# Kernel tuning notes

Measured on AMD Instinct MI355X. Metric: run time of the kernel, lower is better.

## Reference

```python
import jax, jax.numpy as jnp
import numpy as np

BIG, SMALL = 13, 3
NK = 5                       # ceil(BIG / SMALL)
PADDING = SMALL - 1          # 2
EXTRA_PAD = PADDING - SMALL // 2   # 1
G = 2                        # group_in
C_OUT = 96
C_IN = G * C_OUT * NK        # 960
B, H, W = 16, 56, 56


def setup_inputs() -> dict:
    key = jax.random.key(0)
    k1, k2 = jax.random.split(key, 2)
    rng = np.random.default_rng(0)
    mid = BIG // 2
    real_pad = np.array([mid - i * SMALL - PADDING for i in range(NK)], dtype=np.int32)  # [4,1,-2,-5,-8]

    def perm_pads():
        # per output channel, a random permutation of the nk shift offsets
        return np.concatenate([rng.permutation(real_pad) for _ in range(C_OUT)])

    ph = np.stack([perm_pads() for _ in range(G)])  # (G, C_OUT*NK) horizontal shifts
    pv = np.stack([perm_pads() for _ in range(G)])  # (G, C_OUT*NK) vertical shifts
    pad_hv = np.concatenate([ph, pv], axis=0).T.astype(np.int32)  # (C_OUT*NK, 2*G)

    ids = []
    for _ in range(G):
        col = []
        for _ in range(C_OUT):
            arr = -np.ones(NK, dtype=np.int32)
            pos = rng.choice(NK, min(4, NK), replace=False)
            arr[pos] = np.arange(min(4, NK))
            col.append(arr)
        ids.append(np.concatenate(col))
    idx_identit = np.stack(ids).T.astype(np.int32)  # (C_OUT*NK, G)

    x = jax.random.normal(k1, (B, C_IN, H, W), jnp.float32)
    proj_w = jax.random.normal(k2, (C_OUT, C_IN), jnp.float32) * np.float32(1.0 / np.sqrt(C_IN))
    return {
        'x': x,
        'pad_hv': jnp.asarray(pad_hv),
        'idx_identit': jnp.asarray(idx_identit),
        'local_scale': jnp.ones((1, C_IN, 1, 1), jnp.float32),
        'local_bias': jnp.zeros((1, C_IN, 1, 1), jnp.float32),
        'proj_w': proj_w,
        'fuse_alpha': jnp.float32(0.7),
        'b': B, 'hout': H, 'wout': W,
    }


def reference(x, pad_hv, idx_identit, local_scale, local_bias, proj_w, fuse_alpha, b, hout, wout):
    p = EXTRA_PAD
    xp = jnp.pad(x, ((0, 0), (0, 0), (p, p), (p, p)), mode='edge')  # replicate pad
    Bx, Cin, Hp, Wp = xp.shape

    # per-channel shift offsets: channel ic = g*C_OUT*NK + slot, slot = co*NK + k
    ph = pad_hv[:, :G].T.reshape(-1)  # (C_IN,) horizontal (w-axis) shifts
    pv = pad_hv[:, G:].T.reshape(-1)  # (C_IN,) vertical (h-axis) shifts

    def gather_w(xc, s):  # xc: (B, Hp, Wp), s: scalar int shift
        idx = jnp.arange(wout) + p + s
        valid = ((idx >= 0) & (idx < Wp)).astype(xc.dtype)
        return xc[:, p:p + hout, jnp.clip(idx, 0, Wp - 1)] * valid[None, None, :]

    def gather_h(xc, s):
        idx = jnp.arange(hout) + p + s
        valid = ((idx >= 0) & (idx < Hp)).astype(xc.dtype)
        return xc[:, jnp.clip(idx, 0, Hp - 1), p:p + wout] * valid[None, :, None]

    xh = jax.vmap(gather_w, in_axes=(1, 0), out_axes=1)(xp, ph)  # (B, C_IN, hout, wout)
    xv = jax.vmap(gather_h, in_axes=(1, 0), out_axes=1)(xp, pv)
    x1 = xh.reshape(Bx, G, C_OUT, NK, hout, wout).sum((1, 3))    # horizontal-shift group
    x2 = xv.reshape(Bx, G, C_OUT, NK, hout, wout).sum((1, 3))    # vertical-shift group

    id_mask = (idx_identit.T.reshape(-1) >= 0).astype(xp.dtype)  # (C_IN,) identity slots
    x3 = (xp[:, :, p:p + hout, p:p + wout] * id_mask[None, :, None, None])
    x3 = x3.reshape(Bx, G, C_OUT, NK, hout, wout).sum((1, 3))    # identity group

    global_feat = (x1 + x2 + x3) / 3.0

    local = xp * (local_scale + 1e-5) + local_bias
    local = jax.image.resize(local, (Bx, Cin, hout, wout), method='bilinear')  # align_corners=False
    local = jnp.einsum('bchw,oc->bohw', local, proj_w)  # 1x1 conv, no bias

    return fuse_alpha * global_feat + (1.0 - fuse_alpha) * local
```

## Files before the change

kernel.cpp:

```cpp
#include <hip/hip_runtime.h>
#include <hip/hip_bf16.h>
#include <cstdint>
#include <cstddef>

#define B_    16
#define CIN   960
#define HH    56
#define WW_   56
#define GG    2
#define COUT  96
#define NK_   5
#define PIX   3136
#define NCH   30

#define WF_OFF   0
#define BIAS_OFF 61440
#define Y_OFF    61568

typedef __attribute__((ext_vector_type(8))) short bf16x8;
typedef __attribute__((ext_vector_type(4))) float f32x4;

__device__ __forceinline__ short f2b(float f) {
    union { float f; unsigned u; } c; c.f = f;
    unsigned r = (c.u + 0x7FFFu + ((c.u >> 16) & 1u)) >> 16;
    return (short)r;
}
__device__ __forceinline__ float b2f(short s) {
    union { unsigned u; float f; } c;
    c.u = ((unsigned)(unsigned short)s) << 16;
    return c.f;
}

#define GLOAD_LDS16(gp, lp)                                                        \
    __builtin_amdgcn_global_load_lds(                                              \
        (const __attribute__((address_space(1))) unsigned*)(gp),                   \
        (__attribute__((address_space(3))) unsigned*)(lp), 16, 0, 0)

__global__ void prep_wb(const float* __restrict__ pw, const float* __restrict__ sc,
                        short* __restrict__ wf) {
    int idx = blockIdx.x * 256 + threadIdx.x;
    if (idx >= NCH * 6 * 64) return;
    const int lane = idx & 63;
    const int nf   = idx >> 6;
    const int f    = nf % 6;
    const int n    = nf / 6;
    const int o    = f * 16 + (lane & 15);
    const int c0   = n * 32 + (lane >> 4) * 8;
    bf16x8 v;
#pragma unroll
    for (int k = 0; k < 8; ++k)
        v[k] = f2b(pw[o * CIN + c0 + k] * (sc[c0 + k] + 1e-5f));
    *(bf16x8*)((char*)wf + (size_t)n * 8192 + (f * 64 + lane) * 16) = v;
}

__global__ void prep_bias(const float* __restrict__ pw, const float* __restrict__ bi,
                          float* __restrict__ bias) {
    const int o = blockIdx.x;
    const int l = threadIdx.x;
    float s = 0.f;
    for (int c = l; c < CIN; c += 64) s += pw[o * CIN + c] * bi[c];
#pragma unroll
    for (int off = 32; off; off >>= 1) s += __shfl_down(s, off);
    if (l == 0) bias[o] = s;
}

__global__ __launch_bounds__(512)
void conv_mfma(const float* __restrict__ x, const short* __restrict__ wf,
               short* __restrict__ yb) {
    const int tid  = threadIdx.x;
    const int lane = tid & 63;
    const int wv   = tid >> 6;
    const int m    = wv >> 2;
    const int n    = wv & 3;
    const int b    = blockIdx.y;
    const int px0  = blockIdx.x * 64;

    __shared__ __align__(16) char xsb[3 * 8192];
    __shared__ __align__(16) char wlb[3 * 8192];

    const float* xbase = x + (size_t)b * CIN * PIX + px0;
    const char*  wfB   = (const char*)wf;

    const int sch  = wv * 4 + (lane >> 4);
    const int sS   = (wv >> 1) & 3;
    const int soff = (((lane >> 2) & 3) ^ sS) * 16 + (lane & 3) * 4;
    const int wsub = wv * 1024 + lane * 16;

    const int kb    = lane >> 4;
    const int bcol  = (lane & 15) * 4;
    const int bslot = ((n ^ kb) & 3) * 64;
    const int babs  = kb * 2048 + bslot + bcol;
    const int abase = m * 3072 + lane * 16;

    f32x4 acc0 = {0.f, 0.f, 0.f, 0.f};
    f32x4 acc1 = {0.f, 0.f, 0.f, 0.f};
    f32x4 acc2 = {0.f, 0.f, 0.f, 0.f};

#define STAGE(BS, c0)                                                            \
    {                                                                            \
        GLOAD_LDS16(xbase + (size_t)((c0) + sch) * PIX + soff,                   \
                    xsb + (BS) * 8192 + wv * 1024);                              \
        GLOAD_LDS16(wfB + (size_t)((c0) >> 5) * 8192 + wsub,                     \
                    wlb + (BS) * 8192 + wv * 1024);                              \
    }

    STAGE(0, 0);
    STAGE(1, 32);

#define STEP(n_, BI, BS, VM)                                                     \
    {                                                                            \
        asm volatile("s_waitcnt vmcnt(" #VM ")" ::: "memory");                   \
        asm volatile("s_barrier" ::: "memory");                                  \
        bf16x8 bfrag;                                                            \
        _Pragma("unroll")                                                        \
        for (int k = 0; k < 8; ++k)                                              \
            bfrag[k] = f2b(*(const float*)(xsb + (BI) * 8192 + babs + k * 256)); \
        const bf16x8 af0 = *(const bf16x8*)(wlb + (BI) * 8192 + abase);          \
        const bf16x8 af1 = *(const bf16x8*)(wlb + (BI) * 8192 + abase + 1024);   \
        const bf16x8 af2 = *(const bf16x8*)(wlb + (BI) * 8192 + abase + 2048);   \
        if ((n_) + 2 < NCH) STAGE(BS, ((n_) + 2) * 32);                          \
        acc0 = __builtin_amdgcn_mfma_f32_16x16x32_bf16(af0, bfrag, acc0, 0,0,0); \
        acc1 = __builtin_amdgcn_mfma_f32_16x16x32_bf16(af1, bfrag, acc1, 0,0,0); \
        acc2 = __builtin_amdgcn_mfma_f32_16x16x32_bf16(af2, bfrag, acc2, 0,0,0); \
    }

#pragma unroll 1
    for (int mm = 0; mm < 9; ++mm) {
        const int n0 = mm * 3;
        STEP(n0 + 0, 0, 2, 2);
        STEP(n0 + 1, 1, 0, 2);
        STEP(n0 + 2, 2, 1, 2);
    }
    STEP(27, 0, 2, 2);
    STEP(28, 1, 0, 2);
    STEP(29, 2, 1, 0);
#undef STEP
#undef STAGE

    short* yp = yb + (size_t)b * COUT * PIX + px0 + n * 16 + (lane & 15);
    const int o0 = m * 48 + (lane >> 4) * 4;
#pragma unroll
    for (int r = 0; r < 4; ++r) yp[(size_t)(o0 +      r) * PIX] = f2b(acc0[r]);
#pragma unroll
    for (int r = 0; r < 4; ++r) yp[(size_t)(o0 + 16 + r) * PIX] = f2b(acc1[r]);
#pragma unroll
    for (int r = 0; r < 4; ++r) yp[(size_t)(o0 + 32 + r) * PIX] = f2b(acc2[r]);
}

__device__ __forceinline__ void rweights56(int o, short* idx, float* wt) {
    const float ratio = 58.0f / 56.0f;
    const float kinv  = 56.0f / 58.0f;
    const float sf = ((float)o + 0.5f) * ratio - 0.5f;
    const int f0 = (int)floorf(sf);
    float sum = 0.f;
#pragma unroll
    for (int t = 0; t < 4; ++t) {
        int i = f0 - 1 + t;
        float w = fmaxf(1.0f - fabsf(sf - (float)i) * kinv, 0.0f);
        if (i < 0 || i > 57) w = 0.0f;
        idx[t] = (short)min(HH - 1, max(0, i - 1));
        wt[t] = w;
        sum += w;
    }
    const float inv = 1.0f / sum;
#pragma unroll
    for (int t = 0; t < 4; ++t) wt[t] *= inv;
}

__global__ __launch_bounds__(256)
void finalize(const float* __restrict__ x, const int* __restrict__ pad_hv,
              const int* __restrict__ idt, const short* __restrict__ yb,
              const float* __restrict__ bias, const float* __restrict__ alpha_p,
              float* __restrict__ out) {
    const int bc = blockIdx.x;
    const int co = bc % COUT;
    const int b  = bc / COUT;
    const int t  = threadIdx.x;

    __shared__ float  ylds[PIX];
    __shared__ float4 wt4[56];
    __shared__ short4 id4[56];
    __shared__ int   ish[10], isv[10], ipl[10];
    __shared__ float fid[10];

    if (t < 10) {
        const int g = t / 5;
        const int k = t - g * 5;
        const int slot = co * NK_ + k;
        ish[t] = pad_hv[slot * 4 + g];
        isv[t] = pad_hv[slot * 4 + 2 + g];
        fid[t] = (idt[slot * 2 + g] >= 0) ? 1.f : 0.f;
        ipl[t] = (g * (COUT * NK_) + slot) * PIX;
    }
    if (t < 56) {
        short ii[4]; float ww[4];
        rweights56(t, ii, ww);
        wt4[t] = make_float4(ww[0], ww[1], ww[2], ww[3]);
        id4[t] = make_short4(ii[0], ii[1], ii[2], ii[3]);
    }
    {
        const short* yp = yb + (size_t)bc * PIX;
#pragma unroll 1
        for (int i = t; i < PIX / 4; i += 256) {
            const short4 s4 = *(const short4*)(yp + i * 4);
            *(float4*)(ylds + i * 4) =
                make_float4(b2f(s4.x), b2f(s4.y), b2f(s4.z), b2f(s4.w));
        }
    }
    __syncthreads();

    int   ish_r[10], isv_r[10], ipl_r[10];
    float fid_r[10];
#pragma unroll
    for (int p = 0; p < 10; ++p) {
        ish_r[p] = ish[p]; isv_r[p] = isv[p];
        ipl_r[p] = ipl[p]; fid_r[p] = fid[p];
    }

    const float alpha = alpha_p[0];
    const float ia    = 1.0f - alpha;
    const float bco   = bias[co];
    const float* xb = x + (size_t)b * CIN * PIX;
    float* op = out + (size_t)bc * PIX;

#pragma unroll 1
    for (int px = t; px < PIX; px += 256) {
        const int h = (px * 18725) >> 20;
        const int w = px - h * WW_;
        const int hrow = px - w;

        float accg = 0.f;
#pragma unroll
        for (int p = 0; p < 10; ++p) {
            const float* xc = xb + ipl_r[p];
            const int jw = w + ish_r[p];
            const float mh = (jw >= -1 && jw <= WW_) ? 1.f : 0.f;
            accg += mh * xc[hrow + min(WW_ - 1, max(0, jw))];

            const int iv = h + isv_r[p];
            const float mv = (iv >= -1 && iv <= HH) ? 1.f : 0.f;
            accg += mv * xc[min(HH - 1, max(0, iv)) * WW_ + w];

            accg += fid_r[p] * xc[px];
        }

        const float4 ww4 = wt4[w];
        const short4 iw4 = id4[w];
        const float4 wh4 = wt4[h];
        const short4 ih4 = id4[h];
        float accl = 0.f;
#pragma unroll
        for (int a = 0; a < 4; ++a) {
            const int row = ((const short*)&ih4)[a] * WW_;
            const float* yr = ylds + row;
            float rs;
            rs = ww4.x * yr[iw4.x];
            rs = fmaf(ww4.y, yr[iw4.y], rs);
            rs = fmaf(ww4.z, yr[iw4.z], rs);
            rs = fmaf(ww4.w, yr[iw4.w], rs);
            accl = fmaf(((const float*)&wh4)[a], rs, accl);
        }
        accl += bco;

        op[px] = alpha * accg * (1.0f / 3.0f) + ia * accl;
    }
}

extern "C" void kernel_launch(void* const* d_in, const int* in_sizes, int n_in,
                              void* d_out, int out_size, void* d_ws, size_t ws_size,
                              hipStream_t stream) {
    const float* x      = (const float*)d_in[0];
    const int*   pad_hv = (const int*)d_in[1];
    const int*   idt    = (const int*)d_in[2];
    const float* lsc    = (const float*)d_in[3];
    const float* lbi    = (const float*)d_in[4];
    const float* pw     = (const float*)d_in[5];
    const float* alpha  = (const float*)d_in[6];
    float* out = (float*)d_out;

    float* ws   = (float*)d_ws;
    short* wf   = (short*)(ws + WF_OFF);
    float* bias = ws + BIAS_OFF;
    short* yb   = (short*)(ws + Y_OFF);

    prep_wb<<<(NCH * 6 * 64 + 255) / 256, 256, 0, stream>>>(pw, lsc, wf);
    prep_bias<<<COUT, 64, 0, stream>>>(pw, lbi, bias);
    conv_mfma<<<dim3(PIX / 64, B_), 512, 0, stream>>>(x, wf, yb);
    finalize<<<B_ * COUT, 256, 0, stream>>>(x, pad_hv, idt, yb, bias, alpha, out);
}
```

Before: 93.50 us.

## Register-prefetch x, convert once to bf16 in LDS, double-buffer 64-channel phases

```diff
diff --git a/kernel.cpp b/kernel.cpp
--- a/kernel.cpp
+++ b/kernel.cpp
@@ -12,6 +12,7 @@
 #define NK_   5
 #define PIX   3136
 #define NCH   30
+#define NPH   15
 
 #define WF_OFF   0
 #define BIAS_OFF 61440
@@ -75,67 +76,83 @@
     const int b    = blockIdx.y;
     const int px0  = blockIdx.x * 64;
 
-    __shared__ __align__(16) char xsb[3 * 8192];
-    __shared__ __align__(16) char wlb[3 * 8192];
-
-    const float* xbase = x + (size_t)b * CIN * PIX + px0;
+    __shared__ __align__(16) char xls[2 * 8192];
+    __shared__ __align__(16) char wls[2 * 16384];
+
+    const float* xbase = x + (size_t)b * CIN * PIX + px0 + lane;
     const char*  wfB   = (const char*)wf;
 
-    const int sch  = wv * 4 + (lane >> 4);
-    const int sS   = (wv >> 1) & 3;
-    const int soff = (((lane >> 2) & 3) ^ sS) * 16 + (lane & 3) * 4;
-    const int wsub = wv * 1024 + lane * 16;
-
-    const int kb    = lane >> 4;
-    const int bcol  = (lane & 15) * 4;
-    const int bslot = ((n ^ kb) & 3) * 64;
-    const int babs  = kb * 2048 + bslot + bcol;
+    const int ssub = (wv >> 2) * 4096 + (wv & 3) * 1024 + lane * 16;
+    const int sc0  = (wv >> 2) * 32 + (wv & 3) * 8;
+    const int bbase = (lane >> 4) * 1024 + (n * 16 + (lane & 15)) * 16;
     const int abase = m * 3072 + lane * 16;
 
     f32x4 acc0 = {0.f, 0.f, 0.f, 0.f};
     f32x4 acc1 = {0.f, 0.f, 0.f, 0.f};
     f32x4 acc2 = {0.f, 0.f, 0.f, 0.f};
 
-#define STAGE(BS, c0)                                                            \
-    {                                                                            \
-        GLOAD_LDS16(xbase + (size_t)((c0) + sch) * PIX + soff,                   \
-                    xsb + (BS) * 8192 + wv * 1024);                              \
-        GLOAD_LDS16(wfB + (size_t)((c0) >> 5) * 8192 + wsub,                     \
-                    wlb + (BS) * 8192 + wv * 1024);                              \
-    }
-
-    STAGE(0, 0);
-    STAGE(1, 32);
-
-#define STEP(n_, BI, BS, VM)                                                     \
-    {                                                                            \
-        asm volatile("s_waitcnt vmcnt(" #VM ")" ::: "memory");                   \
-        asm volatile("s_barrier" ::: "memory");                                  \
-        bf16x8 bfrag;                                                            \
+    float vA[8], vB[8];
+
+#define XLOAD(DST, P)                                                            \
+    {                                                                            \
         _Pragma("unroll")                                                        \
         for (int k = 0; k < 8; ++k)                                              \
-            bfrag[k] = f2b(*(const float*)(xsb + (BI) * 8192 + babs + k * 256)); \
-        const bf16x8 af0 = *(const bf16x8*)(wlb + (BI) * 8192 + abase);          \
-        const bf16x8 af1 = *(const bf16x8*)(wlb + (BI) * 8192 + abase + 1024);   \
-        const bf16x8 af2 = *(const bf16x8*)(wlb + (BI) * 8192 + abase + 2048);   \
-        if ((n_) + 2 < NCH) STAGE(BS, ((n_) + 2) * 32);                          \
-        acc0 = __builtin_amdgcn_mfma_f32_16x16x32_bf16(af0, bfrag, acc0, 0,0,0); \
-        acc1 = __builtin_amdgcn_mfma_f32_16x16x32_bf16(af1, bfrag, acc1, 0,0,0); \
-        acc2 = __builtin_amdgcn_mfma_f32_16x16x32_bf16(af2, bfrag, acc2, 0,0,0); \
-    }
+            DST[k] = xbase[(size_t)((P) * 64 + sc0 + k) * PIX];                  \
+    }
+#define WLOAD(P)                                                                 \
+    {                                                                            \
+        _Pragma("unroll")                                                        \
+        for (int s = 0; s < 2; ++s)                                              \
+            GLOAD_LDS16(wfB + (size_t)(2 * (P) + s) * 8192 + wv * 1024 + lane * 16, \
+                        wls + ((P) & 1) * 16384 + s * 8192 + wv * 1024);         \
+    }
+#define PACKWRITE(CUR, P)                                                        \
+    {                                                                            \
+        bf16x8 pk;                                                               \
+        _Pragma("unroll")                                                        \
+        for (int k = 0; k < 8; ++k) pk[k] = f2b(CUR[k]);                         \
+        *(bf16x8*)(xls + ((P) & 1) * 8192 + ssub) = pk;                          \
+    }
+#define COMPUTE(P)                                                               \
+    {                                                                            \
+        _Pragma("unroll")                                                        \
+        for (int s = 0; s < 2; ++s) {                                            \
+            const bf16x8 bf = *(const bf16x8*)(xls + ((P) & 1) * 8192 + s * 4096 + bbase); \
+            const char* wb_ = wls + ((P) & 1) * 16384 + s * 8192 + abase;        \
+            const bf16x8 a0 = *(const bf16x8*)(wb_);                             \
+            const bf16x8 a1 = *(const bf16x8*)(wb_ + 1024);                      \
+            const bf16x8 a2 = *(const bf16x8*)(wb_ + 2048);                      \
+            acc0 = __builtin_amdgcn_mfma_f32_16x16x32_bf16(a0, bf, acc0, 0,0,0); \
+            acc1 = __builtin_amdgcn_mfma_f32_16x16x32_bf16(a1, bf, acc1, 0,0,0); \
+            acc2 = __builtin_amdgcn_mfma_f32_16x16x32_bf16(a2, bf, acc2, 0,0,0); \
+        }                                                                        \
+    }
+#define PHASE(P, CUR, NXT, VM, ISSUE)                                            \
+    {                                                                            \
+        if (ISSUE) XLOAD(NXT, (P) + 1);                                          \
+        asm volatile("s_waitcnt vmcnt(" #VM ")" ::: "memory");                   \
+        PACKWRITE(CUR, P);                                                       \
+        asm volatile("s_waitcnt lgkmcnt(0)" ::: "memory");                       \
+        asm volatile("s_barrier" ::: "memory");                                  \
+        if (ISSUE) WLOAD((P) + 1);                                               \
+        COMPUTE(P);                                                              \
+    }
+
+    XLOAD(vA, 0);
+    WLOAD(0);
 
 #pragma unroll 1
-    for (int mm = 0; mm < 9; ++mm) {
-        const int n0 = mm * 3;
-        STEP(n0 + 0, 0, 2, 2);
-        STEP(n0 + 1, 1, 0, 2);
-        STEP(n0 + 2, 2, 1, 2);
-    }
-    STEP(27, 0, 2, 2);
-    STEP(28, 1, 0, 2);
-    STEP(29, 2, 1, 0);
-#undef STEP
-#undef STAGE
+    for (int pp = 0; pp < 7; ++pp) {
+        const int p0 = pp * 2;
+        PHASE(p0 + 0, vA, vB, 8, 1);
+        PHASE(p0 + 1, vB, vA, 8, 1);
+    }
+    PHASE(14, vA, vB, 0, 0);
+#undef PHASE
+#undef COMPUTE
+#undef PACKWRITE
+#undef WLOAD
+#undef XLOAD
 
     short* yp = yb + (size_t)b * COUT * PIX + px0 + n * 16 + (lane & 15);
     const int o0 = m * 48 + (lane >> 4) * 4;
```

Result: slower. 102.1 us (+9.2%).

## Replace LDS-staged triple buffering with direct register double-buffered global loads

Applied to the files above, without the earlier changes.

```diff
diff --git a/kernel.cpp b/kernel.cpp
--- a/kernel.cpp
+++ b/kernel.cpp
@@ -30,11 +30,6 @@
     c.u = ((unsigned)(unsigned short)s) << 16;
     return c.f;
 }
-
-#define GLOAD_LDS16(gp, lp)                                                        \
-    __builtin_amdgcn_global_load_lds(                                              \
-        (const __attribute__((address_space(1))) unsigned*)(gp),                   \
-        (__attribute__((address_space(3))) unsigned*)(lp), 16, 0, 0)
 
 __global__ void prep_wb(const float* __restrict__ pw, const float* __restrict__ sc,
                         short* __restrict__ wf) {
@@ -75,67 +70,59 @@
     const int b    = blockIdx.y;
     const int px0  = blockIdx.x * 64;
 
-    __shared__ __align__(16) char xsb[3 * 8192];
-    __shared__ __align__(16) char wlb[3 * 8192];
-
-    const float* xbase = x + (size_t)b * CIN * PIX + px0;
-    const char*  wfB   = (const char*)wf;
-
-    const int sch  = wv * 4 + (lane >> 4);
-    const int sS   = (wv >> 1) & 3;
-    const int soff = (((lane >> 2) & 3) ^ sS) * 16 + (lane & 3) * 4;
-    const int wsub = wv * 1024 + lane * 16;
-
-    const int kb    = lane >> 4;
-    const int bcol  = (lane & 15) * 4;
-    const int bslot = ((n ^ kb) & 3) * 64;
-    const int babs  = kb * 2048 + bslot + bcol;
-    const int abase = m * 3072 + lane * 16;
+    const float* xpx = x + (size_t)b * CIN * PIX + px0 + n * 16 + (lane & 15);
+    const int kb8 = (lane >> 4) * 8;
+    const char* wfl = (const char*)wf + m * 3072 + lane * 16;
 
     f32x4 acc0 = {0.f, 0.f, 0.f, 0.f};
     f32x4 acc1 = {0.f, 0.f, 0.f, 0.f};
     f32x4 acc2 = {0.f, 0.f, 0.f, 0.f};
 
-#define STAGE(BS, c0)                                                            \
+    float  xA[8], xB[8];
+    bf16x8 wA0, wA1, wA2, wB0, wB1, wB2;
+
+#define LOADX(DST, N)                                                            \
     {                                                                            \
-        GLOAD_LDS16(xbase + (size_t)((c0) + sch) * PIX + soff,                   \
-                    xsb + (BS) * 8192 + wv * 1024);                              \
-        GLOAD_LDS16(wfB + (size_t)((c0) >> 5) * 8192 + wsub,                     \
-                    wlb + (BS) * 8192 + wv * 1024);                              \
-    }
-
-    STAGE(0, 0);
-    STAGE(1, 32);
-
-#define STEP(n_, BI, BS, VM)                                                     \
-    {                                                                            \
-        asm volatile("s_waitcnt vmcnt(" #VM ")" ::: "memory");                   \
-        asm volatile("s_barrier" ::: "memory");                                  \
-        bf16x8 bfrag;                                                            \
         _Pragma("unroll")                                                        \
         for (int k = 0; k < 8; ++k)                                              \
-            bfrag[k] = f2b(*(const float*)(xsb + (BI) * 8192 + babs + k * 256)); \
-        const bf16x8 af0 = *(const bf16x8*)(wlb + (BI) * 8192 + abase);          \
-        const bf16x8 af1 = *(const bf16x8*)(wlb + (BI) * 8192 + abase + 1024);   \
-        const bf16x8 af2 = *(const bf16x8*)(wlb + (BI) * 8192 + abase + 2048);   \
-        if ((n_) + 2 < NCH) STAGE(BS, ((n_) + 2) * 32);                          \
-        acc0 = __builtin_amdgcn_mfma_f32_16x16x32_bf16(af0, bfrag, acc0, 0,0,0); \
-        acc1 = __builtin_amdgcn_mfma_f32_16x16x32_bf16(af1, bfrag, acc1, 0,0,0); \
-        acc2 = __builtin_amdgcn_mfma_f32_16x16x32_bf16(af2, bfrag, acc2, 0,0,0); \
-    }
+            DST[k] = xpx[(size_t)((N) * 32 + kb8 + k) * PIX];                    \
+    }
+#define LOADW(D0, D1, D2, N)                                                     \
+    {                                                                            \
+        const char* wp_ = wfl + (size_t)(N) * 8192;                              \
+        D0 = *(const bf16x8*)(wp_);                                              \
+        D1 = *(const bf16x8*)(wp_ + 1024);                                       \
+        D2 = *(const bf16x8*)(wp_ + 2048);                                       \
+    }
+#define COMP(XV, W0, W1, W2)                                                     \
+    {                                                                            \
+        bf16x8 bf;                                                               \
+        _Pragma("unroll")                                                        \
+        for (int k = 0; k < 8; ++k) bf[k] = f2b(XV[k]);                          \
+        acc0 = __builtin_amdgcn_mfma_f32_16x16x32_bf16(W0, bf, acc0, 0, 0, 0);   \
+        acc1 = __builtin_amdgcn_mfma_f32_16x16x32_bf16(W1, bf, acc1, 0, 0, 0);   \
+        acc2 = __builtin_amdgcn_mfma_f32_16x16x32_bf16(W2, bf, acc2, 0, 0, 0);   \
+    }
+
+    LOADX(xA, 0);
+    LOADW(wA0, wA1, wA2, 0);
 
 #pragma unroll 1
-    for (int mm = 0; mm < 9; ++mm) {
-        const int n0 = mm * 3;
-        STEP(n0 + 0, 0, 2, 2);
-        STEP(n0 + 1, 1, 0, 2);
-        STEP(n0 + 2, 2, 1, 2);
-    }
-    STEP(27, 0, 2, 2);
-    STEP(28, 1, 0, 2);
-    STEP(29, 2, 1, 0);
-#undef STEP
-#undef STAGE
+    for (int p = 0; p < 14; ++p) {
+        LOADX(xB, 2 * p + 1);
+        LOADW(wB0, wB1, wB2, 2 * p + 1);
+        COMP(xA, wA0, wA1, wA2);
+        LOADX(xA, 2 * p + 2);
+        LOADW(wA0, wA1, wA2, 2 * p + 2);
+        COMP(xB, wB0, wB1, wB2);
+    }
+    LOADX(xB, 29);
+    LOADW(wB0, wB1, wB2, 29);
+    COMP(xA, wA0, wA1, wA2);
+    COMP(xB, wB0, wB1, wB2);
+#undef COMP
+#undef LOADW
+#undef LOADX
 
     short* yp = yb + (size_t)b * COUT * PIX + px0 + n * 16 + (lane & 15);
     const int o0 = m * 48 + (lane >> 4) * 4;
```

Result: slower. 121.0 us (+29.4%).

## Load activations to registers, convert once to bf16 in LDS, DMA weights separately

Applied to the files above, without the earlier changes.

```diff
diff --git a/kernel.cpp b/kernel.cpp
--- a/kernel.cpp
+++ b/kernel.cpp
@@ -75,67 +75,84 @@
     const int b    = blockIdx.y;
     const int px0  = blockIdx.x * 64;
 
-    __shared__ __align__(16) char xsb[3 * 8192];
-    __shared__ __align__(16) char wlb[3 * 8192];
-
-    const float* xbase = x + (size_t)b * CIN * PIX + px0;
-    const char*  wfB   = (const char*)wf;
-
-    const int sch  = wv * 4 + (lane >> 4);
-    const int sS   = (wv >> 1) & 3;
-    const int soff = (((lane >> 2) & 3) ^ sS) * 16 + (lane & 3) * 4;
+    __shared__ __align__(16) char xls[2 * 4096];
+    __shared__ __align__(16) char wls[3 * 8192];
+
+    const int skb = wv >> 1;
+    const int sh8 = (wv & 1) * 8;
+    const float* xsrc = x + (size_t)b * CIN * PIX + px0 + lane
+                        + (size_t)(skb * 8 + (wv & 1) * 4) * PIX;
+    const int wxb = skb * 1024 + lane * 16 + sh8;
+    const char* wfB = (const char*)wf;
     const int wsub = wv * 1024 + lane * 16;
 
-    const int kb    = lane >> 4;
-    const int bcol  = (lane & 15) * 4;
-    const int bslot = ((n ^ kb) & 3) * 64;
-    const int babs  = kb * 2048 + bslot + bcol;
-    const int abase = m * 3072 + lane * 16;
+    const int bbyte = (lane >> 4) * 1024 + (n * 16 + (lane & 15)) * 16;
+    const int abyte = m * 3072 + lane * 16;
 
     f32x4 acc0 = {0.f, 0.f, 0.f, 0.f};
     f32x4 acc1 = {0.f, 0.f, 0.f, 0.f};
     f32x4 acc2 = {0.f, 0.f, 0.f, 0.f};
 
-#define STAGE(BS, c0)                                                            \
+    float vX0[4], vX1[4], vX2[4];
+
+#define XLOAD(D, N)                                                              \
     {                                                                            \
-        GLOAD_LDS16(xbase + (size_t)((c0) + sch) * PIX + soff,                   \
-                    xsb + (BS) * 8192 + wv * 1024);                              \
-        GLOAD_LDS16(wfB + (size_t)((c0) >> 5) * 8192 + wsub,                     \
-                    wlb + (BS) * 8192 + wv * 1024);                              \
-    }
-
-    STAGE(0, 0);
-    STAGE(1, 32);
-
-#define STEP(n_, BI, BS, VM)                                                     \
+        _Pragma("unroll")                                                        \
+        for (int k = 0; k < 4; ++k)                                              \
+            D[k] = xsrc[(size_t)((N) * 32 + k) * PIX];                           \
+    }
+#define WDMA(N, DB)                                                              \
+    GLOAD_LDS16(wfB + (size_t)(N) * 8192 + wsub, wls + (DB) * 8192 + wv * 1024);
+
+#define STEP(n_, XBI, WBI, WDN, RCUR, RNXT, VM, ISSUE)                           \
     {                                                                            \
+        if (ISSUE) XLOAD(RNXT, (n_) + 2);                                        \
         asm volatile("s_waitcnt vmcnt(" #VM ")" ::: "memory");                   \
+        {                                                                        \
+            short4 pk;                                                           \
+            pk.x = f2b(RCUR[0]); pk.y = f2b(RCUR[1]);                            \
+            pk.z = f2b(RCUR[2]); pk.w = f2b(RCUR[3]);                            \
+            *(short4*)(xls + (XBI) * 4096 + wxb) = pk;                           \
+        }                                                                        \
+        asm volatile("s_waitcnt lgkmcnt(0)" ::: "memory");                       \
         asm volatile("s_barrier" ::: "memory");                                  \
-        bf16x8 bfrag;                                                            \
-        _Pragma("unroll")                                                        \
-        for (int k = 0; k < 8; ++k)                                              \
-            bfrag[k] = f2b(*(const float*)(xsb + (BI) * 8192 + babs + k * 256)); \
-        const bf16x8 af0 = *(const bf16x8*)(wlb + (BI) * 8192 + abase);          \
-        const bf16x8 af1 = *(const bf16x8*)(wlb + (BI) * 8192 + abase + 1024);   \
-        const bf16x8 af2 = *(const bf16x8*)(wlb + (BI) * 8192 + abase + 2048);   \
-        if ((n_) + 2 < NCH) STAGE(BS, ((n_) + 2) * 32);                          \
-        acc0 = __builtin_amdgcn_mfma_f32_16x16x32_bf16(af0, bfrag, acc0, 0,0,0); \
-        acc1 = __builtin_amdgcn_mfma_f32_16x16x32_bf16(af1, bfrag, acc1, 0,0,0); \
-        acc2 = __builtin_amdgcn_mfma_f32_16x16x32_bf16(af2, bfrag, acc2, 0,0,0); \
-    }
+        if (ISSUE) WDMA((n_) + 2, WDN);                                          \
+        {                                                                        \
+            const bf16x8 bf = *(const bf16x8*)(xls + (XBI) * 4096 + bbyte);      \
+            const char* wp_ = wls + (WBI) * 8192 + abyte;                        \
+            const bf16x8 a0 = *(const bf16x8*)(wp_);                             \
+            const bf16x8 a1 = *(const bf16x8*)(wp_ + 1024);                      \
+            const bf16x8 a2 = *(const bf16x8*)(wp_ + 2048);                      \
+            acc0 = __builtin_amdgcn_mfma_f32_16x16x32_bf16(a0, bf, acc0, 0,0,0); \
+            acc1 = __builtin_amdgcn_mfma_f32_16x16x32_bf16(a1, bf, acc1, 0,0,0); \
+            acc2 = __builtin_amdgcn_mfma_f32_16x16x32_bf16(a2, bf, acc2, 0,0,0); \
+        }                                                                        \
+    }
+
+    XLOAD(vX0, 0);
+    WDMA(0, 0);
+    XLOAD(vX1, 1);
+    WDMA(1, 1);
 
 #pragma unroll 1
-    for (int mm = 0; mm < 9; ++mm) {
-        const int n0 = mm * 3;
-        STEP(n0 + 0, 0, 2, 2);
-        STEP(n0 + 1, 1, 0, 2);
-        STEP(n0 + 2, 2, 1, 2);
-    }
-    STEP(27, 0, 2, 2);
-    STEP(28, 1, 0, 2);
-    STEP(29, 2, 1, 0);
+    for (int mm = 0; mm < 4; ++mm) {
+        const int n0 = mm * 6;
+        STEP(n0 + 0, 0, 0, 2, vX0, vX2, 9, 1);
+        STEP(n0 + 1, 1, 1, 0, vX1, vX0, 9, 1);
+        STEP(n0 + 2, 0, 2, 1, vX2, vX1, 9, 1);
+        STEP(n0 + 3, 1, 0, 2, vX0, vX2, 9, 1);
+        STEP(n0 + 4, 0, 1, 0, vX1, vX0, 9, 1);
+        STEP(n0 + 5, 1, 2, 1, vX2, vX1, 9, 1);
+    }
+    STEP(24, 0, 0, 2, vX0, vX2, 9, 1);
+    STEP(25, 1, 1, 0, vX1, vX0, 9, 1);
+    STEP(26, 0, 2, 1, vX2, vX1, 9, 1);
+    STEP(27, 1, 0, 2, vX0, vX2, 9, 1);
+    STEP(28, 0, 1, 0, vX1, vX1, 5, 0);
+    STEP(29, 1, 2, 1, vX2, vX2, 0, 0);
 #undef STEP
-#undef STAGE
+#undef WDMA
+#undef XLOAD
 
     short* yp = yb + (size_t)b * COUT * PIX + px0 + n * 16 + (lane & 15);
     const int o0 = m * 48 + (lane >> 4) * 4;
```

New measurement: 101.8 us. 1.09x slower.
